# Kernel optimization log

Hardware: AMD Instinct MI355X
Metric: run time of the kernel (lower is better)

Reference implementation:

```python
import jax, jax.numpy as jnp
import numpy as np

D = 1024      # d_model
H = 16        # n_heads
M = 64        # n_memories
DK = D // H   # head dim
EPS = 1e-5    # LayerNorm eps


def setup_inputs() -> dict:
    key = jax.random.key(0)
    ks = jax.random.split(key, 16)
    B, N = 4, 1024
    s = 0.02
    return {
        "queries": jax.random.normal(ks[0], (B, N, D), jnp.float32),
        "keys": jax.random.normal(ks[1], (B, N, D), jnp.float32),
        "values": jax.random.normal(ks[2], (B, N, D), jnp.float32),
        "attention_mask": jax.random.randint(ks[3], (B, 1, 1, N), 0, 2, dtype=jnp.int32),
        "Wq": jax.random.normal(ks[4], (D, D), jnp.float32) * s,
        "bq": jnp.zeros((D,), jnp.float32),
        "Wk": jax.random.normal(ks[5], (D, D), jnp.float32) * s,
        "bk": jnp.zeros((D,), jnp.float32),
        "Wv": jax.random.normal(ks[6], (D, D), jnp.float32) * s,
        "bv": jnp.zeros((D,), jnp.float32),
        "Wo": jax.random.normal(ks[7], (D, D), jnp.float32) * s,
        "bo": jnp.zeros((D,), jnp.float32),
        "m_k": jax.random.normal(ks[8], (1, M, D), jnp.float32) * 0.01,
        "m_v": jax.random.normal(ks[9], (1, M, D), jnp.float32) * 0.01,
        "gamma": jnp.ones((D,), jnp.float32),
        "beta": jnp.zeros((D,), jnp.float32),
    }


def _layer_norm(x, gamma, beta):
    mu = jnp.mean(x, axis=-1, keepdims=True)
    var = jnp.var(x, axis=-1, keepdims=True)
    return (x - mu) * jax.lax.rsqrt(var + EPS) * gamma + beta


def reference(queries, keys, values, attention_mask,
              Wq, bq, Wk, bk, Wv, bv, Wo, bo, m_k, m_v, gamma, beta):
    B, Nq, _ = queries.shape
    Nk = keys.shape[1]
    scale = 1.0 / np.sqrt(DK)

    # projections (torch Linear: x @ W.T + b)
    q = (queries @ Wq.T + bq).reshape(B, Nq, H, DK).transpose(0, 2, 1, 3)  # b h nq d

    # memory-augmented K/V (memory tokens scaled as in the source)
    k_full = jnp.concatenate(
        [keys @ Wk.T + bk, jnp.broadcast_to(m_k * np.sqrt(DK), (B, M, D))], axis=1)
    v_full = jnp.concatenate(
        [values @ Wv.T + bv, jnp.broadcast_to(m_v * np.sqrt(M), (B, M, D))], axis=1)
    k = k_full.reshape(B, Nk + M, H, DK).transpose(0, 2, 1, 3)  # b h nk+m d
    v = v_full.reshape(B, Nk + M, H, DK).transpose(0, 2, 1, 3)  # b h nk+m d

    scores = jnp.einsum('bhqd,bhkd->bhqk', q, k) * scale  # [B,H,Nq,Nk+M]

    # partial masking: only the first Nk (non-memory) columns are maskable
    mask = jnp.concatenate(
        [attention_mask.astype(bool),
         jnp.zeros((B, 1, 1, M), dtype=bool)], axis=-1)
    scores = jnp.where(mask, -jnp.inf, scores)

    p_attn = jax.nn.softmax(scores, axis=-1)  # dropout p=0.0 -> identity
    out = jnp.einsum('bhqk,bhkd->bhqd', p_attn, v)
    out = out.transpose(0, 2, 1, 3).reshape(B, Nq, D)
    out = out @ Wo.T + bo

    # residual + LayerNorm (outer dropout is identity at p=0.0)
    return _layer_norm(queries + out, gamma, beta)
```

## Files before the change

### kernel.cpp

```cpp
#include <hip/hip_runtime.h>


typedef __bf16 bf16;
typedef __bf16 bf16x8 __attribute__((ext_vector_type(8)));
typedef __bf16 bf16x4 __attribute__((ext_vector_type(4)));
typedef __bf16 bf16x2 __attribute__((ext_vector_type(2)));
typedef float  f32x4  __attribute__((ext_vector_type(4)));
typedef float  f32x16 __attribute__((ext_vector_type(16)));
typedef unsigned uintx4 __attribute__((ext_vector_type(4)));

#define NSEQ 1024
#define NKV  1088
#define DMODEL 1024

struct CvtArgs { const float* s[7]; const float* mk; const float* mv; };

__global__ __launch_bounds__(256) void prep(CvtArgs c, bf16* __restrict__ dst,
                                            bf16* __restrict__ Kb,
                                            bf16* __restrict__ Vt)
{
    int blk = blockIdx.x;
    if (blk < 8192) {
        size_t e = ((size_t)blk * 256 + threadIdx.x) * 8;
        const float* s;
        if (e < ((size_t)3 << 22)) {
            s = c.s[e >> 22] + (e & 0x3FFFFF);
        } else {
            size_t wq = e - ((size_t)3 << 22);
            s = c.s[3 + (wq >> 20)] + (wq & 0xFFFFF);
        }
        f32x4 a = *(const f32x4*)s;
        f32x4 b = *(const f32x4*)(s + 4);
        bf16x8 o;
        for (int i = 0; i < 4; i++) { o[i] = (bf16)a[i]; o[4 + i] = (bf16)b[i]; }
        *(bf16x8*)&dst[e] = o;
    } else {
        int i = (blk - 8192) * 256 + threadIdx.x;
        int b = i >> 16, md = i & 65535;
        int m = md >> 10, dcol = md & 1023;
        Kb[(size_t)b * (NKV * DMODEL) + (size_t)(NSEQ + m) * DMODEL + dcol]
            = (bf16)(c.mk[md] * 8.0f);
        Vt[((size_t)b * 1024 + dcol) * NKV + NSEQ + m] = (bf16)(c.mv[md] * 8.0f);
    }
}

typedef __attribute__((address_space(1))) void gas_void;
typedef __attribute__((address_space(3))) void las_void;

__device__ __forceinline__ void gload16(const bf16* g, bf16* l)
{
    __builtin_amdgcn_global_load_lds((gas_void*)g, (las_void*)l, 16, 0, 0);
}

struct GemmArgsB {
    const bf16* A;
    const bf16* W;
    const float* bias;
    bf16* C;
    int osK;
    int vt;
};

__global__ __launch_bounds__(256, 3) void gemm128_lds(GemmArgsB g0, GemmArgsB g1,
                                                      GemmArgsB g2)
{
    const GemmArgsB g = (blockIdx.z == 0) ? g0 : (blockIdx.z == 1) ? g1 : g2;
    __shared__ bf16 As[128][32];
    __shared__ bf16 Bs[128][32];
    const int t = threadIdx.x;
    const int lane = t & 63, w = t >> 6;
    const int qi = lane & 15, qq = lane >> 4;
    const int wrow = (w >> 1) * 64, wcol = (w & 1) * 64;
    const int bm = blockIdx.y * 128, bn = blockIdx.x * 128;

    const int srow = w * 32 + (lane >> 2);
    const int scol = (lane & 3) * 8;
    const bf16* Ag = g.A + (size_t)(bm + srow) * DMODEL + scol;
    const bf16* Wg = g.W + (size_t)(bn + srow) * DMODEL + scol;
    bf16* Al = &As[w * 32][0];
    bf16* Bl = &Bs[w * 32][0];

    f32x4 acc[4][4] = {};

#define STAGE(kt)                                                             \
    do {                                                                      \
        gload16(Ag + (kt),                 Al);                               \
        gload16(Ag + (kt) + 16 * DMODEL,   Al + 16 * 32);                     \
        gload16(Wg + (kt),                 Bl);                               \
        gload16(Wg + (kt) + 16 * DMODEL,   Bl + 16 * 32);                    \
    } while (0)

    STAGE(0);
    for (int kt = 0; kt < DMODEL; kt += 32) {
        __syncthreads();
        bf16x8 a[4], b[4];
        for (int i = 0; i < 4; i++)
            a[i] = *(const bf16x8*)&As[wrow + i * 16 + qi][qq * 8];
        for (int j = 0; j < 4; j++)
            b[j] = *(const bf16x8*)&Bs[wcol + j * 16 + qi][qq * 8];
        __syncthreads();
        if (kt + 32 < DMODEL) STAGE(kt + 32);
        for (int i = 0; i < 4; i++)
            for (int j = 0; j < 4; j++)
                acc[i][j] = __builtin_amdgcn_mfma_f32_16x16x32_bf16(
                    a[i], b[j], acc[i][j], 0, 0, 0);
    }
#undef STAGE

    for (int i = 0; i < 4; i++)
        for (int j = 0; j < 4; j++) {
            int row0 = bm + wrow + i * 16 + qq * 4;
            int col  = bn + wcol + j * 16 + qi;
            float bcol = g.bias[col];
            if (g.vt) {
                bf16x4 v;
                for (int r = 0; r < 4; r++) v[r] = (bf16)(acc[i][j][r] + bcol);
                size_t off = ((size_t)((row0 >> 10) * 16 + (col >> 6)) * 64 + (col & 63))
                           * NKV + (row0 & 1023);
                *(bf16x4*)&g.C[off] = v;
            } else {
                for (int r = 0; r < 4; r++) {
                    int row = row0 + r;
                    size_t off = (size_t)(row >> 10) * g.osK
                               + (size_t)(row & 1023) * DMODEL + col;
                    g.C[off] = (bf16)(acc[i][j][r] + bcol);
                }
            }
        }
}

struct GemmArgs {
    const void* A;
    const float* W;
    const float* bias;
    bf16* C;
    int osK;
    int vt;
};

template<bool ABF>
__global__ __launch_bounds__(256, 2) void gemm128(GemmArgs g0, GemmArgs g1, GemmArgs g2)
{
    const GemmArgs g = (blockIdx.z == 0) ? g0 : (blockIdx.z == 1) ? g1 : g2;
    __shared__ bf16 As[128][44];
    __shared__ bf16 Bs[128][44];
    const int t = threadIdx.x;
    const int lane = t & 63, w = t >> 6;
    const int qi = lane & 15, qq = lane >> 4;
    const int wrow = (w >> 1) * 64, wcol = (w & 1) * 64;
    const int bm = blockIdx.y * 128, bn = blockIdx.x * 128;
    const int sr = t >> 1, sc = (t & 1) * 16;

    f32x4 acc[4][4] = {};

    f32x4 pa[4];
    bf16x8 pab[2];
    f32x4 pw[4];

    const float* Wp = g.W + (size_t)(bn + sr) * DMODEL + sc;
    const float* Af = (const float*)g.A + (size_t)(bm + sr) * DMODEL + sc;
    const bf16*  Ab = (const bf16*)g.A + (size_t)(bm + sr) * DMODEL + sc;

#define LOAD_TILES(kt)                                                        \
    do {                                                                      \
        if (ABF) {                                                            \
            pab[0] = *(const bf16x8*)(Ab + (kt));                             \
            pab[1] = *(const bf16x8*)(Ab + (kt) + 8);                         \
        } else {                                                              \
            pa[0] = *(const f32x4*)(Af + (kt));                               \
            pa[1] = *(const f32x4*)(Af + (kt) + 4);                           \
            pa[2] = *(const f32x4*)(Af + (kt) + 8);                           \
            pa[3] = *(const f32x4*)(Af + (kt) + 12);                          \
        }                                                                     \
        pw[0] = *(const f32x4*)(Wp + (kt));                                   \
        pw[1] = *(const f32x4*)(Wp + (kt) + 4);                               \
        pw[2] = *(const f32x4*)(Wp + (kt) + 8);                               \
        pw[3] = *(const f32x4*)(Wp + (kt) + 12);                              \
    } while (0)

#define STORE_TILES()                                                         \
    do {                                                                      \
        if (ABF) {                                                            \
            *(bf16x8*)&As[sr][sc]     = pab[0];                               \
            *(bf16x8*)&As[sr][sc + 8] = pab[1];                               \
        } else {                                                              \
            bf16x8 v0, v1;                                                    \
            for (int i = 0; i < 4; i++) {                                     \
                v0[i] = (bf16)pa[0][i]; v0[4 + i] = (bf16)pa[1][i];           \
                v1[i] = (bf16)pa[2][i]; v1[4 + i] = (bf16)pa[3][i];           \
            }                                                                 \
            *(bf16x8*)&As[sr][sc]     = v0;                                   \
            *(bf16x8*)&As[sr][sc + 8] = v1;                                   \
        }                                                                     \
        {                                                                     \
            bf16x8 u0, u1;                                                    \
            for (int i = 0; i < 4; i++) {                                     \
                u0[i] = (bf16)pw[0][i]; u0[4 + i] = (bf16)pw[1][i];           \
                u1[i] = (bf16)pw[2][i]; u1[4 + i] = (bf16)pw[3][i];           \
            }                                                                 \
            *(bf16x8*)&Bs[sr][sc]     = u0;                                   \
            *(bf16x8*)&Bs[sr][sc + 8] = u1;                                   \
        }                                                                     \
    } while (0)

    LOAD_TILES(0);
    STORE_TILES();
    __syncthreads();

    for (int kt = 0; kt < DMODEL; kt += 32) {
        const bool more = (kt + 32) < DMODEL;
        if (more) LOAD_TILES(kt + 32);
        bf16x8 a[4], b[4];
        for (int i = 0; i < 4; i++)
            a[i] = *(const bf16x8*)&As[wrow + i * 16 + qi][qq * 8];
        for (int j = 0; j < 4; j++)
            b[j] = *(const bf16x8*)&Bs[wcol + j * 16 + qi][qq * 8];
        for (int i = 0; i < 4; i++)
            for (int j = 0; j < 4; j++)
                acc[i][j] = __builtin_amdgcn_mfma_f32_16x16x32_bf16(a[i], b[j], acc[i][j], 0, 0, 0);
        if (more) {
            __syncthreads();
            STORE_TILES();
            __syncthreads();
        }
    }
#undef LOAD_TILES
#undef STORE_TILES

    for (int i = 0; i < 4; i++)
        for (int j = 0; j < 4; j++) {
            int row0 = bm + wrow + i * 16 + qq * 4;
            int col  = bn + wcol + j * 16 + qi;
            float bcol = g.bias[col];
            if (g.vt) {
                bf16x4 v;
                for (int r = 0; r < 4; r++) v[r] = (bf16)(acc[i][j][r] + bcol);
                size_t off = ((size_t)((row0 >> 10) * 16 + (col >> 6)) * 64 + (col & 63))
                           * NKV + (row0 & 1023);
                *(bf16x4*)&g.C[off] = v;
            } else {
                for (int r = 0; r < 4; r++) {
                    int row = row0 + r;
                    size_t off = (size_t)(row >> 10) * g.osK
                               + (size_t)(row & 1023) * DMODEL + col;
                    g.C[off] = (bf16)(acc[i][j][r] + bcol);
                }
            }
        }
}

__global__ void fill_mem(const float* __restrict__ mk, const float* __restrict__ mv,
                         bf16* __restrict__ K, bf16* __restrict__ Vt)
{
    int i = blockIdx.x * 256 + threadIdx.x;
    int b = i >> 16, md = i & 65535;
    int m = md >> 10, dcol = md & 1023;
    K[(size_t)b * (NKV * DMODEL) + (size_t)(NSEQ + m) * DMODEL + dcol]
        = (bf16)(mk[md] * 8.0f);
    Vt[((size_t)b * 1024 + dcol) * NKV + NSEQ + m] = (bf16)(mv[md] * 8.0f);
}

__device__ __forceinline__ unsigned pkbf(float a, float b)
{
    bf16x2 t; t[0] = (bf16)a; t[1] = (bf16)b;
    unsigned u; __builtin_memcpy(&u, &t, 4); return u;
}

__global__ __launch_bounds__(256) void attn_flash(const bf16* Q,
        const bf16* __restrict__ K, const bf16* __restrict__ Vt,
        const int* __restrict__ mask, bf16* O)
{
    __shared__ bf16 sKV[2][2][64][72];
    __shared__ __align__(16) float sM[NKV];
    const int t = threadIdx.x, lane = t & 63, w = t >> 6;
    int bh, q0;
    if (gridDim.y == 64) {
        int lin = blockIdx.y * gridDim.x + blockIdx.x;
        bh = ((lin & 7) << 3) | ((lin >> 3) & 7);
        q0 = (lin >> 6) * 128;
    } else {
        bh = blockIdx.y;
        q0 = blockIdx.x * 128;
    }
    const int b = bh >> 4, h = bh & 15;
    const int sr = t >> 2, sc = (t & 3) * 16;
    const int lq = lane & 31, hi = lane >> 5;

    for (int j = t; j < NKV; j += 256)
        sM[j] = (j < NSEQ && mask[b * NSEQ + j] != 0) ? -3.0e38f : 0.0f;

    const size_t qrow = (size_t)(b * NSEQ + q0 + w * 32 + lq) * DMODEL + h * 64;
    bf16x8 qf[4];
#pragma unroll
    for (int c = 0; c < 4; c++) {
        bf16x8 v = *(const bf16x8*)&Q[qrow + c * 16 + hi * 8];
        for (int i = 0; i < 8; i++) v[i] = (bf16)((float)v[i] * 0.125f);
        qf[c] = v;
    }

    const bf16* kbase = K + (size_t)(b * NKV + sr) * DMODEL + h * 64 + sc;
    const bf16* vbase = Vt + ((size_t)bh * 64 + sr) * NKV + sc;

    bf16x8 pk0, pk1, pv0, pv1;
#define LOAD_KV(jt)                                                           \
    do {                                                                      \
        const bf16* kp = kbase + (size_t)(jt) * 64 * DMODEL;                  \
        pk0 = *(const bf16x8*)kp;                                             \
        pk1 = *(const bf16x8*)(kp + 8);                                       \
        const bf16* vp = vbase + (jt) * 64;                                   \
        pv0 = *(const bf16x8*)vp;                                             \
        pv1 = *(const bf16x8*)(vp + 8);                                       \
    } while (0)
#define STORE_KV(bi)                                                          \
    do {                                                                      \
        *(bf16x8*)&sKV[bi][0][sr][sc]     = pk0;                              \
        *(bf16x8*)&sKV[bi][0][sr][sc + 8] = pk1;                              \
        *(bf16x8*)&sKV[bi][1][sr][sc]     = pv0;                              \
        *(bf16x8*)&sKV[bi][1][sr][sc + 8] = pv1;                              \
    } while (0)

    LOAD_KV(0);
    STORE_KV(0);

    float m_i = -1.0e30f, l_i = 0.f;
    f32x16 oacc0 = {}, oacc1 = {};

    for (int jt = 0; jt < 17; jt++) {
        const int j0 = jt * 64;
        const int cb = jt & 1;
        const bool more = jt < 16;
        if (more) LOAD_KV(jt + 1);
        __syncthreads();

        f32x16 accs[2];
#pragma unroll
        for (int kb = 0; kb < 2; kb++) {
#pragma unroll
            for (int g2 = 0; g2 < 4; g2++) {
                f32x4 m4 = *(const f32x4*)&sM[j0 + kb * 32 + 8 * g2 + 4 * hi];
                accs[kb][4 * g2 + 0] = m4[0];
                accs[kb][4 * g2 + 1] = m4[1];
                accs[kb][4 * g2 + 2] = m4[2];
                accs[kb][4 * g2 + 3] = m4[3];
            }
#pragma unroll
            for (int c = 0; c < 4; c++) {
                bf16x8 kf = *(const bf16x8*)&sKV[cb][0][kb * 32 + lq][c * 16 + hi * 8];
                accs[kb] = __builtin_amdgcn_mfma_f32_32x32x16_bf16(
                    kf, qf[c], accs[kb], 0, 0, 0);
            }
        }

        float rm0 = accs[0][0], rm1 = accs[1][0];
#pragma unroll
        for (int r = 1; r < 16; r++) {
            rm0 = fmaxf(rm0, accs[0][r]);
            rm1 = fmaxf(rm1, accs[1][r]);
        }
        float rm = fmaxf(rm0, rm1);
        rm = fmaxf(rm, __shfl_xor(rm, 32, 64));
        if (!__all(rm - m_i <= 8.0f)) {
            float mnew = fmaxf(m_i, rm);
            float alpha = __expf(m_i - mnew);
            m_i = mnew;
            l_i *= alpha;
#pragma unroll
            for (int r = 0; r < 16; r++) { oacc0[r] *= alpha; oacc1[r] *= alpha; }
        }
        float rs0 = 0.f, rs1 = 0.f;
#pragma unroll
        for (int r = 0; r < 16; r++) {
            float p0 = __expf(accs[0][r] - m_i);
            float p1 = __expf(accs[1][r] - m_i);
            accs[0][r] = p0; accs[1][r] = p1;
            rs0 += p0; rs1 += p1;
        }
        float rs = rs0 + rs1;
        rs += __shfl_xor(rs, 32, 64);
        l_i += rs;

        unsigned dwv[16];
#pragma unroll
        for (int kb = 0; kb < 2; kb++)
#pragma unroll
            for (int a = 0; a < 4; a++) {
                dwv[kb * 8 + 2 * a]     = pkbf(accs[kb][4 * a], accs[kb][4 * a + 1]);
                dwv[kb * 8 + 2 * a + 1] = pkbf(accs[kb][4 * a + 2], accs[kb][4 * a + 3]);
            }
        bf16x8 pb[4];
#pragma unroll
        for (int c = 0; c < 4; c++) {
            const int base = (c >> 1) * 8 + (c & 1) * 4;
            unsigned e0 = dwv[base],     e1 = dwv[base + 1];
            unsigned o0 = dwv[base + 2], o1 = dwv[base + 3];
            uintx4 cw;
#if __has_builtin(__builtin_amdgcn_permlane32_swap)
            auto r0 = __builtin_amdgcn_permlane32_swap(e0, o0, false, false);
            auto r1 = __builtin_amdgcn_permlane32_swap(e1, o1, false, false);
            cw[0] = r0[0]; cw[1] = r1[0]; cw[2] = r0[1]; cw[3] = r1[1];
#else
            unsigned s0 = hi ? e0 : o0, s1 = hi ? e1 : o1;
            unsigned k0 = hi ? o0 : e0, k1 = hi ? o1 : e1;
            unsigned x0 = __shfl_xor((int)s0, 32, 64);
            unsigned x1 = __shfl_xor((int)s1, 32, 64);
            cw[0] = hi ? x0 : k0; cw[1] = hi ? x1 : k1;
            cw[2] = hi ? k0 : x0; cw[3] = hi ? k1 : x1;
#endif
            __builtin_memcpy(&pb[c], &cw, 16);
        }

#pragma unroll
        for (int c = 0; c < 4; c++) {
            bf16x8 vf0 = *(const bf16x8*)&sKV[cb][1][lq][c * 16 + hi * 8];
            bf16x8 vf1 = *(const bf16x8*)&sKV[cb][1][32 + lq][c * 16 + hi * 8];
            oacc0 = __builtin_amdgcn_mfma_f32_32x32x16_bf16(vf0, pb[c], oacc0, 0, 0, 0);
            oacc1 = __builtin_amdgcn_mfma_f32_32x32x16_bf16(vf1, pb[c], oacc1, 0, 0, 0);
        }
        if (more) STORE_KV(cb ^ 1);
    }
#undef LOAD_KV
#undef STORE_KV

    float linv = 1.0f / l_i;
    __syncthreads();
    bf16 (*sO)[72] = reinterpret_cast<bf16(*)[72]>(&sKV[0][0][0][0]);
#pragma unroll
    for (int r = 0; r < 16; r++) {
        int dl = (r & 3) + 8 * (r >> 2) + 4 * hi;
        sO[w * 32 + lq][dl]      = (bf16)(oacc0[r] * linv);
        sO[w * 32 + lq][32 + dl] = (bf16)(oacc1[r] * linv);
    }
    __syncthreads();
    {
        int row = t >> 1, ch = (t & 1) * 32;
        bf16* dst = &O[(size_t)(b * NSEQ + q0 + row) * DMODEL + h * 64 + ch];
#pragma unroll
        for (int k = 0; k < 4; k++)
            *(bf16x8*)(dst + k * 8) = *(const bf16x8*)&sO[row][ch + k * 8];
    }
}

__global__ __launch_bounds__(256) void residual_ln(const float* __restrict__ X,
        const bf16* __restrict__ Y, const float* __restrict__ gamma,
        const float* __restrict__ beta, float* __restrict__ out)
{
    __shared__ float red[8];
    int row = blockIdx.x, t = threadIdx.x;
    size_t base = (size_t)row * DMODEL + t * 4;
    f32x4  xv = *(const f32x4*)&X[base];
    bf16x4 yv = *(const bf16x4*)&Y[base];
    float s[4], sum = 0.f, sq = 0.f;
    for (int i = 0; i < 4; i++) {
        s[i] = xv[i] + (float)yv[i];
        sum += s[i]; sq += s[i] * s[i];
    }
    for (int o = 32; o; o >>= 1) { sum += __shfl_xor(sum, o, 64); sq += __shfl_xor(sq, o, 64); }
    if ((t & 63) == 0) { red[t >> 6] = sum; red[4 + (t >> 6)] = sq; }
    __syncthreads();
    sum = red[0] + red[1] + red[2] + red[3];
    sq  = red[4] + red[5] + red[6] + red[7];
    float mean = sum * (1.0f / DMODEL);
    float var  = sq  * (1.0f / DMODEL) - mean * mean;
    float rstd = rsqrtf(var + 1e-5f);
    f32x4 gv = *(const f32x4*)&gamma[t * 4];
    f32x4 bv = *(const f32x4*)&beta[t * 4];
    f32x4 ov;
    for (int i = 0; i < 4; i++)
        ov[i] = (s[i] - mean) * rstd * gv[i] + bv[i];
    *(f32x4*)&out[base] = ov;
}

extern "C" void kernel_launch(void* const* d_in, const int* in_sizes, int n_in,
                              void* d_out, int out_size, void* d_ws, size_t ws_size,
                              hipStream_t stream)
{
    const float* queries = (const float*)d_in[0];
    const float* keys    = (const float*)d_in[1];
    const float* values  = (const float*)d_in[2];
    const int*   amask   = (const int*)d_in[3];
    const float* Wq = (const float*)d_in[4];  const float* bq = (const float*)d_in[5];
    const float* Wk = (const float*)d_in[6];  const float* bk = (const float*)d_in[7];
    const float* Wv = (const float*)d_in[8];  const float* bv = (const float*)d_in[9];
    const float* Wo = (const float*)d_in[10]; const float* bo = (const float*)d_in[11];
    const float* mk = (const float*)d_in[12]; const float* mv = (const float*)d_in[13];
    const float* gamma = (const float*)d_in[14]; const float* beta = (const float*)d_in[15];
    float* out = (float*)d_out;

    bf16* Qb = (bf16*)(out + (size_t)2 * 1024 * 1024);
    const size_t SB  = (size_t)NSEQ * DMODEL;
    const size_t KVB = (size_t)NKV * DMODEL;
    dim3 gb(256);

    const size_t need_r10 = (2 * 4 * KVB + 3 * 4 * SB + 4 * SB) * sizeof(bf16);

    if (ws_size >= need_r10) {
        bf16* Kb = (bf16*)d_ws;
        bf16* Vt = Kb + 4 * KVB;
        bf16* Ab = Vt + 4 * KVB;
        bf16* Wb = Ab + 12 * SB;
        bf16* PR = Ab;

        CvtArgs ca;
        ca.s[0] = queries; ca.s[1] = keys; ca.s[2] = values;
        ca.s[3] = Wq; ca.s[4] = Wk; ca.s[5] = Wv; ca.s[6] = Wo;
        ca.mk = mk; ca.mv = mv;
        prep<<<dim3(8192 + 1024), gb, 0, stream>>>(ca, Ab, Kb, Vt);

        GemmArgsB gq{Ab,           Wb,           bq, Qb, (int)SB,  0};
        GemmArgsB gk{Ab + 4 * SB,  Wb + SB,      bk, Kb, (int)KVB, 0};
        GemmArgsB gv{Ab + 8 * SB,  Wb + 2 * SB,  bv, Vt, 0,        1};
        gemm128_lds<<<dim3(8, 32, 3), gb, 0, stream>>>(gq, gk, gv);
        attn_flash<<<dim3(8, 64), gb, 0, stream>>>(Qb, Kb, Vt, amask, Qb);
        GemmArgsB go{Qb, Wb + 3 * SB, bo, PR, (int)SB, 0};
        gemm128_lds<<<dim3(8, 32, 1), gb, 0, stream>>>(go, go, go);
        residual_ln<<<dim3(4096), gb, 0, stream>>>(queries, PR, gamma, beta, out);
    } else if (ws_size >= (size_t)2 * 4 * KVB * sizeof(bf16)) {
        bf16* Kb = (bf16*)d_ws;
        bf16* Vt = Kb + 4 * KVB;
        bf16* PR = Kb;

        GemmArgs gq{queries, Wq, bq, Qb, (int)SB,  0};
        GemmArgs gk{keys,    Wk, bk, Kb, (int)KVB, 0};
        GemmArgs gv{values,  Wv, bv, Vt, 0,        1};
        gemm128<false><<<dim3(8, 32, 3), gb, 0, stream>>>(gq, gk, gv);
        fill_mem<<<dim3(1024), gb, 0, stream>>>(mk, mv, Kb, Vt);
        attn_flash<<<dim3(8, 64), gb, 0, stream>>>(Qb, Kb, Vt, amask, Qb);
        GemmArgs go{Qb, Wo, bo, PR, (int)SB, 0};
        gemm128<true><<<dim3(8, 32, 1), gb, 0, stream>>>(go, go, go);
        residual_ln<<<dim3(4096), gb, 0, stream>>>(queries, PR, gamma, beta, out);
    } else {
        bf16* Kb = (bf16*)d_ws;
        bf16* Vt = Kb + KVB;
        bf16* PR = Kb;

        GemmArgs gq{queries, Wq, bq, Qb, (int)SB, 0};
        gemm128<false><<<dim3(8, 32, 1), gb, 0, stream>>>(gq, gq, gq);
        for (int b = 0; b < 4; b++) {
            GemmArgs gk{keys   + b * SB, Wk, bk, Kb, 0, 0};
            GemmArgs gv{values + b * SB, Wv, bv, Vt, 0, 1};
            gemm128<false><<<dim3(8, 8, 2), gb, 0, stream>>>(gk, gv, gv);
            fill_mem<<<dim3(256), gb, 0, stream>>>(mk, mv, Kb, Vt);
            attn_flash<<<dim3(8, 16), gb, 0, stream>>>(Qb + b * SB, Kb, Vt,
                                                       amask + b * NSEQ, Qb + b * SB);
            GemmArgs go{Qb + b * SB, Wo, bo, PR, 0, 0};
            gemm128<true><<<dim3(8, 8, 1), gb, 0, stream>>>(go, go, go);
            residual_ln<<<dim3(1024), gb, 0, stream>>>(queries + b * SB, PR,
                                                       gamma, beta, out + b * SB);
        }
    }
}
```

Before: 229.6 us.

## Fuse fp32-to-bf16 prep and QKV GEMM into one cooperative kernel with grid sync

Merges the conversion/memory-fill kernel and the QKV projection GEMM into a single cooperative launch of 768 blocks. The blocks first do the conversion in a grid-stride loop, then meet at a grid-wide barrier, then each runs one GEMM tile. This is meant to remove one kernel launch and the gap between the two kernels. In exchange it adds the cost of the grid barrier, ties the conversion to the GEMM's occupancy, and keeps a fallback to the two separate kernels if the cooperative launch fails.

Result: slower. 376.7 us (+64.0%).

```diff
diff --git a/kernel.cpp b/kernel.cpp
--- a/kernel.cpp
+++ b/kernel.cpp
@@ -1,4 +1,7 @@
 #include <hip/hip_runtime.h>
+#include <hip/hip_cooperative_groups.h>
+
+namespace cg = cooperative_groups;
 
 
 typedef __bf16 bf16;
@@ -15,32 +18,42 @@
 
 struct CvtArgs { const float* s[7]; const float* mk; const float* mv; };
 
+__device__ __forceinline__ void cvt_one(const CvtArgs& c, bf16* __restrict__ dst,
+                                        size_t e)
+{
+    const float* s;
+    if (e < ((size_t)3 << 22)) {
+        s = c.s[e >> 22] + (e & 0x3FFFFF);
+    } else {
+        size_t wq = e - ((size_t)3 << 22);
+        s = c.s[3 + (wq >> 20)] + (wq & 0xFFFFF);
+    }
+    f32x4 a = *(const f32x4*)s;
+    f32x4 b = *(const f32x4*)(s + 4);
+    bf16x8 o;
+    for (int i = 0; i < 4; i++) { o[i] = (bf16)a[i]; o[4 + i] = (bf16)b[i]; }
+    *(bf16x8*)&dst[e] = o;
+}
+
+__device__ __forceinline__ void fill_one(const CvtArgs& c, bf16* __restrict__ Kb,
+                                         bf16* __restrict__ Vt, int i)
+{
+    int b = i >> 16, md = i & 65535;
+    int m = md >> 10, dcol = md & 1023;
+    Kb[(size_t)b * (NKV * DMODEL) + (size_t)(NSEQ + m) * DMODEL + dcol]
+        = (bf16)(c.mk[md] * 8.0f);
+    Vt[((size_t)b * 1024 + dcol) * NKV + NSEQ + m] = (bf16)(c.mv[md] * 8.0f);
+}
+
 __global__ __launch_bounds__(256) void prep(CvtArgs c, bf16* __restrict__ dst,
                                             bf16* __restrict__ Kb,
                                             bf16* __restrict__ Vt)
 {
     int blk = blockIdx.x;
     if (blk < 8192) {
-        size_t e = ((size_t)blk * 256 + threadIdx.x) * 8;
-        const float* s;
-        if (e < ((size_t)3 << 22)) {
-            s = c.s[e >> 22] + (e & 0x3FFFFF);
-        } else {
-            size_t wq = e - ((size_t)3 << 22);
-            s = c.s[3 + (wq >> 20)] + (wq & 0xFFFFF);
-        }
-        f32x4 a = *(const f32x4*)s;
-        f32x4 b = *(const f32x4*)(s + 4);
-        bf16x8 o;
-        for (int i = 0; i < 4; i++) { o[i] = (bf16)a[i]; o[4 + i] = (bf16)b[i]; }
-        *(bf16x8*)&dst[e] = o;
+        cvt_one(c, dst, ((size_t)blk * 256 + threadIdx.x) * 8);
     } else {
-        int i = (blk - 8192) * 256 + threadIdx.x;
-        int b = i >> 16, md = i & 65535;
-        int m = md >> 10, dcol = md & 1023;
-        Kb[(size_t)b * (NKV * DMODEL) + (size_t)(NSEQ + m) * DMODEL + dcol]
-            = (bf16)(c.mk[md] * 8.0f);
-        Vt[((size_t)b * 1024 + dcol) * NKV + NSEQ + m] = (bf16)(c.mv[md] * 8.0f);
+        fill_one(c, Kb, Vt, (blk - 8192) * 256 + threadIdx.x);
     }
 }
 
@@ -61,17 +74,15 @@
     int vt;
 };
 
-__global__ __launch_bounds__(256, 3) void gemm128_lds(GemmArgsB g0, GemmArgsB g1,
-                                                      GemmArgsB g2)
-{
-    const GemmArgsB g = (blockIdx.z == 0) ? g0 : (blockIdx.z == 1) ? g1 : g2;
+__device__ __forceinline__ void gemm128_body(const GemmArgsB g, int bx, int by)
+{
     __shared__ bf16 As[128][32];
     __shared__ bf16 Bs[128][32];
     const int t = threadIdx.x;
     const int lane = t & 63, w = t >> 6;
     const int qi = lane & 15, qq = lane >> 4;
     const int wrow = (w >> 1) * 64, wcol = (w & 1) * 64;
-    const int bm = blockIdx.y * 128, bn = blockIdx.x * 128;
+    const int bm = by * 128, bn = bx * 128;
 
     const int srow = w * 32 + (lane >> 2);
     const int scol = (lane & 3) * 8;
@@ -127,6 +138,31 @@
                 }
             }
         }
+}
+
+__global__ __launch_bounds__(256, 3) void gemm128_lds(GemmArgsB g0, GemmArgsB g1,
+                                                      GemmArgsB g2)
+{
+    const GemmArgsB g = (blockIdx.z == 0) ? g0 : (blockIdx.z == 1) ? g1 : g2;
+    gemm128_body(g, blockIdx.x, blockIdx.y);
+}
+
+__global__ __launch_bounds__(256, 3) void prep_qkv(CvtArgs c, bf16* dstA,
+        bf16* KbP, bf16* VtP, GemmArgsB g0, GemmArgsB g1, GemmArgsB g2)
+{
+    const int gid = blockIdx.x * 256 + threadIdx.x;
+    const int gstride = 768 * 256;
+    for (size_t i8 = gid; i8 < (size_t)2097152; i8 += gstride)
+        cvt_one(c, dstA, i8 * 8);
+    for (int i = gid; i < 262144; i += gstride)
+        fill_one(c, KbP, VtP, i);
+
+    cg::this_grid().sync();
+
+    const int blk = blockIdx.x;
+    const int bz = blk >> 8;
+    const GemmArgsB g = (bz == 0) ? g0 : (bz == 1) ? g1 : g2;
+    gemm128_body(g, blk & 7, (blk >> 3) & 31);
 }
 
 struct GemmArgs {
@@ -504,12 +540,19 @@
         ca.s[0] = queries; ca.s[1] = keys; ca.s[2] = values;
         ca.s[3] = Wq; ca.s[4] = Wk; ca.s[5] = Wv; ca.s[6] = Wo;
         ca.mk = mk; ca.mv = mv;
-        prep<<<dim3(8192 + 1024), gb, 0, stream>>>(ca, Ab, Kb, Vt);
 
         GemmArgsB gq{Ab,           Wb,           bq, Qb, (int)SB,  0};
         GemmArgsB gk{Ab + 4 * SB,  Wb + SB,      bk, Kb, (int)KVB, 0};
         GemmArgsB gv{Ab + 8 * SB,  Wb + 2 * SB,  bv, Vt, 0,        1};
-        gemm128_lds<<<dim3(8, 32, 3), gb, 0, stream>>>(gq, gk, gv);
+
+        void* cargs[] = { &ca, &Ab, &Kb, &Vt, &gq, &gk, &gv };
+        hipError_t ce = hipLaunchCooperativeKernel((void*)prep_qkv,
+                            dim3(768), gb, cargs, 0, stream);
+        if (ce != hipSuccess) {
+            prep<<<dim3(8192 + 1024), gb, 0, stream>>>(ca, Ab, Kb, Vt);
+            gemm128_lds<<<dim3(8, 32, 3), gb, 0, stream>>>(gq, gk, gv);
+        }
+
         attn_flash<<<dim3(8, 64), gb, 0, stream>>>(Qb, Kb, Vt, amask, Qb);
         GemmArgsB go{Qb, Wb + 3 * SB, bo, PR, (int)SB, 0};
         gemm128_lds<<<dim3(8, 32, 1), gb, 0, stream>>>(go, go, go);
```
